# Performance work log

Measured on AMD Instinct MI355X. Metric: run time of the kernel, lower is better.

Reference implementation:

```python
import math
import jax, jax.numpy as jnp
import numpy as np

N_EXPERTS = 8
CAP_FACTOR = 1.25
D_MODEL = 1024
D_FF = 4096
B, T = 8, 2048


def setup_inputs() -> dict:
    key = jax.random.key(0)
    k1, k2, k3, k4 = jax.random.split(key, 4)
    hidden = jax.random.normal(k1, (B, T, D_MODEL), dtype=jnp.float32)
    # router: Linear(d_model, n_experts, bias=False), init std=0.01; store as (D, E)
    router_w = jax.random.normal(k2, (D_MODEL, N_EXPERTS), dtype=jnp.float32) * 0.01
    # per-expert MLP weights stacked: W1 (E, D, F), W2 (E, F, D)
    s1 = 1.0 / math.sqrt(D_MODEL)
    s2 = 1.0 / math.sqrt(D_FF)
    W1 = jax.random.uniform(k3, (N_EXPERTS, D_MODEL, D_FF), dtype=jnp.float32, minval=-s1, maxval=s1)
    W2 = jax.random.uniform(k4, (N_EXPERTS, D_FF, D_MODEL), dtype=jnp.float32, minval=-s2, maxval=s2)
    return {"hidden": hidden, "router_w": router_w, "W1": W1, "W2": W2}


def reference(hidden, router_w, W1, W2):
    Bb, Tt, D = hidden.shape
    N = Bb * Tt
    E = router_w.shape[1]
    capacity = min(int(math.ceil(CAP_FACTOR * N / E)), N)

    hidden_flat = hidden.reshape(N, D)
    logits = hidden_flat @ router_w                 # (N, E)
    router_probs = jax.nn.softmax(logits, axis=-1)  # (N, E)

    scores = router_probs.T                         # (E, N)
    weights, indices = jax.lax.top_k(scores, capacity)  # (E, C) each

    # gather tokens per expert: (E, C, D)
    expert_in = hidden_flat[indices]
    h = jnp.einsum('ecd,edf->ecf', expert_in, W1)
    h = jax.nn.gelu(h, approximate=False)           # torch nn.GELU default (erf)
    expert_out = jnp.einsum('ecf,efd->ecd', h, W2)  # (E, C, D)
    contrib = weights[..., None] * expert_out       # (E, C, D)

    output = jnp.zeros((N, D), dtype=hidden.dtype)
    output = output.at[indices.reshape(-1)].add(contrib.reshape(-1, D))
    output = output.reshape(Bb, Tt, D)

    eps = 1e-8
    entropy = -(router_probs * jnp.log(router_probs + eps)).sum(-1)
    aux_loss = -entropy.mean()
    return output, aux_loss
```

## Files before the change

### kernel.cpp

```cpp
#include <hip/hip_runtime.h>
#include <hip/hip_bf16.h>
#include <math.h>

#define NTOK 16384
#define DM 1024
#define DFF 4096
#define NEXP 8
#define CAP 2560

typedef __bf16 bf16;
typedef float f32x4 __attribute__((ext_vector_type(4)));
typedef bf16 bf16x8 __attribute__((ext_vector_type(8)));
typedef bf16 bf16x4 __attribute__((ext_vector_type(4)));

#define OFF_PROBS 0ull
#define OFF_IDX   524288ull
#define OFF_WTS   606208ull
#define OFF_W1T   688128ull
#define OFF_W2T   67796992ull
#define OFF_X     134905856ull
#define OFF_ENT   OFF_X
#define OFF_H     176848896ull
#define WS_MIN    197820416ull
#define WS_FUSED  344621056ull

#define BAR() do { asm volatile("" ::: "memory"); __builtin_amdgcn_s_barrier(); asm volatile("" ::: "memory"); } while (0)

__device__ __forceinline__ void gl16(const bf16* g, const bf16* l) {
  __builtin_amdgcn_global_load_lds((const __attribute__((address_space(1))) void*)g,
                                   (__attribute__((address_space(3))) void*)l, 16, 0, 0);
}

__device__ __forceinline__ float gelu_f(float x) {
  float u = 1.5957691216057308f * (x + 0.044715f * x * x * x);
  return x * __builtin_amdgcn_rcpf(1.f + __expf(-u));
}

__global__ __launch_bounds__(256) void k_transpose_cvt(const float* __restrict__ src,
                                                       bf16* __restrict__ dst, int R, int C) {
  __shared__ float tile[64][69];
  int e = blockIdx.z;
  src += (size_t)e * R * C;
  dst += (size_t)e * R * C;
  int c0 = blockIdx.x * 64, r0 = blockIdx.y * 64;
  int t = threadIdx.x;
  int tr = t >> 4, tc4 = (t & 15) * 4;
#pragma unroll
  for (int i = 0; i < 4; i++) {
    int r = tr + i * 16;
    float4 v = *(const float4*)(src + (size_t)(r0 + r) * C + c0 + tc4);
    tile[r][tc4] = v.x; tile[r][tc4 + 1] = v.y; tile[r][tc4 + 2] = v.z; tile[r][tc4 + 3] = v.w;
  }
  __syncthreads();
#pragma unroll
  for (int i = 0; i < 4; i++) {
    int orr = tr + i * 16;
    bf16x4 o = {(bf16)tile[tc4][orr], (bf16)tile[tc4 + 1][orr],
                (bf16)tile[tc4 + 2][orr], (bf16)tile[tc4 + 3][orr]};
    *(bf16x4*)(dst + (size_t)(c0 + orr) * R + r0 + tc4) = o;
  }
}

__global__ __launch_bounds__(256) void k_router(const float* __restrict__ hidden,
                                                const float* __restrict__ rw,
                                                float* __restrict__ probsT,
                                                float* __restrict__ entPart) {
  __shared__ float went[4];
  int wv = threadIdx.x >> 6, lane = threadIdx.x & 63;
  int token = blockIdx.x * 4 + wv;
  float acc[NEXP];
#pragma unroll
  for (int e = 0; e < NEXP; e++) acc[e] = 0.f;
  const float* hp = hidden + (size_t)token * DM;
  for (int d = lane; d < DM; d += 64) {
    float h = hp[d];
#pragma unroll
    for (int e = 0; e < NEXP; e++) acc[e] = fmaf(h, rw[d * NEXP + e], acc[e]);
  }
#pragma unroll
  for (int e = 0; e < NEXP; e++) {
    float v = acc[e];
#pragma unroll
    for (int s = 1; s < 64; s <<= 1) v += __shfl_xor(v, s);
    acc[e] = v;
  }
  float mx = acc[0];
#pragma unroll
  for (int e = 1; e < NEXP; e++) mx = fmaxf(mx, acc[e]);
  float p[NEXP], s = 0.f;
#pragma unroll
  for (int e = 0; e < NEXP; e++) { p[e] = expf(acc[e] - mx); s += p[e]; }
  float inv = 1.f / s;
  float ent = 0.f;
#pragma unroll
  for (int e = 0; e < NEXP; e++) { p[e] *= inv; ent += p[e] * logf(p[e] + 1e-8f); }
  if (lane < NEXP) probsT[(size_t)lane * NTOK + token] = p[lane];
  if (lane == 0) went[wv] = ent;
  __syncthreads();
  if (threadIdx.x == 0) entPart[blockIdx.x] = went[0] + went[1] + went[2] + went[3];
}

__global__ __launch_bounds__(256) void k_aux(const float* __restrict__ part, float* __restrict__ outAux) {
  __shared__ float s[256];
  int t = threadIdx.x;
  float v = 0.f;
#pragma unroll
  for (int i = 0; i < 16; i++) v += part[i * 256 + t];
  s[t] = v;
  __syncthreads();
  for (int st = 128; st > 0; st >>= 1) {
    if (t < st) s[t] += s[t + st];
    __syncthreads();
  }
  if (t == 0) outAux[0] = s[0] * (1.f / (float)NTOK);
}

__global__ __launch_bounds__(1024) void k_topk(const float* __restrict__ probsT,
                                               int* __restrict__ idx,
                                               float* __restrict__ wts) {
  int e = blockIdx.x;
  const float* row = probsT + (size_t)e * NTOK;
  int t = threadIdx.x;
  unsigned u[16];
#pragma unroll
  for (int j = 0; j < 16; j++) u[j] = __float_as_uint(row[j * 1024 + t]);
  __shared__ int wred[16];
  __shared__ int bc;
  __shared__ int cnt_gt, cnt_eq;
  __shared__ int eqbuf[2048];
  int lane = t & 63, wv = t >> 6;
  unsigned prefix = 0;
  for (int bit = 30; bit >= 0; bit--) {
    unsigned cand = prefix | (1u << bit);
    int c = 0;
#pragma unroll
    for (int j = 0; j < 16; j++) c += (u[j] >= cand) ? 1 : 0;
#pragma unroll
    for (int s = 1; s < 64; s <<= 1) c += __shfl_xor(c, s);
    if (lane == 0) wred[wv] = c;
    __syncthreads();
    if (t == 0) { int tot = 0; for (int k = 0; k < 16; k++) tot += wred[k]; bc = tot; }
    __syncthreads();
    if (bc >= CAP) prefix = cand;
  }
  unsigned vC = prefix;
  if (t == 0) { cnt_gt = 0; cnt_eq = 0; }
  __syncthreads();
#pragma unroll
  for (int j = 0; j < 16; j++) {
    int i = j * 1024 + t;
    if (u[j] > vC) {
      int p = atomicAdd(&cnt_gt, 1);
      idx[e * CAP + p] = i;
      wts[e * CAP + p] = __uint_as_float(u[j]);
    } else if (u[j] == vC) {
      int p = atomicAdd(&cnt_eq, 1);
      if (p < 2048) eqbuf[p] = i;
    }
  }
  __syncthreads();
  int m = cnt_gt;
  int ne = cnt_eq > 2048 ? 2048 : cnt_eq;
  int needed = CAP - m;
  for (int j = t; j < ne; j += 1024) {
    int my = eqbuf[j];
    int rank = 0;
    for (int k = 0; k < ne; k++) rank += (eqbuf[k] < my) ? 1 : 0;
    if (rank < needed) {
      idx[e * CAP + m + rank] = my;
      wts[e * CAP + m + rank] = __uint_as_float(vC);
    }
  }
}

__global__ void k_gather(const float* __restrict__ hidden, const int* __restrict__ idx,
                         bf16* __restrict__ X) {
  int ec = blockIdx.x;
  int token = idx[ec];
  const float4* src = (const float4*)(hidden + (size_t)token * DM);
  bf16* dstrow = X + (size_t)ec * DM;
  int t = threadIdx.x;
  float4 v = src[t];
  bf16x4 o = {(bf16)v.x, (bf16)v.y, (bf16)v.z, (bf16)v.w};
  *(bf16x4*)(dstrow + t * 4) = o;
}

template <int EPI>
__global__ __launch_bounds__(512, 2) void k_gemm256p(
    const bf16* __restrict__ Ab, const bf16* __restrict__ Bb,
    bf16* __restrict__ Hb, const int* __restrict__ idxb, const float* __restrict__ wtsb,
    float* __restrict__ outb, int serialE) {
  constexpr int KD = (EPI == 0) ? DM : DFF;
  constexpr int NT = (EPI == 0) ? 16 : 32;

  __shared__ bf16 As[2][256 * 64];
  __shared__ bf16 Bs[2][256 * 64];

  int e, slot, nA;
  if (serialE >= 0) { e = serialE; slot = blockIdx.x; nA = 1; }
  else {
    e = blockIdx.x & 7;
    slot = blockIdx.x >> 3;
    nA = (EPI == 0) ? 5 : ((slot < 16) ? 3 : 2);
  }
  const bf16* A = Ab + (size_t)e * ((EPI == 0) ? (size_t)CAP * DM : (size_t)CAP * DFF);
  const bf16* B = Bb + (size_t)e * ((EPI == 0) ? (size_t)DFF * DM : (size_t)DM * DFF);

  int t = threadIdx.x, lane = t & 63, wv = t >> 6;
  int wm = wv >> 2, wn = wv & 3;
  int l3 = lane >> 3, l7 = lane & 7;
  int cswz = (l7 ^ l3) * 8;

  auto decode = [&](int seq, int& m0, int& n0, int& k0) {
    int s_ = seq / 40, r_ = seq % 40;
    int bx = r_ >> 2, q = r_ & 3;
    m0 = bx * 256;
    if constexpr (EPI == 0) { n0 = (s_ * 4 + q) * 256; k0 = 0; }
    else { n0 = q * 256; k0 = s_ * 2048; }
  };

  auto stage = [&](const bf16* Am, const bf16* Bn, int half, int ktE, int buf) {
#pragma unroll
    for (int j = 0; j < 2; ++j) {
      int u = wv * 2 + j;
      int rb; const bf16* G; bf16* L;
      if (half == 0)      { rb = u * 8 + (u >> 3) * 64;            G = Am + (size_t)(rb + l3) * KD; L = &As[buf][rb * 64]; }
      else if (half == 3) { rb = 64 + u * 8 + (u >> 3) * 64;       G = Am + (size_t)(rb + l3) * KD; L = &As[buf][rb * 64]; }
      else if (half == 1) { rb = (u >> 2) * 64 + (u & 3) * 8;      G = Bn + (size_t)(rb + l3) * KD; L = &Bs[buf][rb * 64]; }
      else                { rb = (u >> 2) * 64 + 32 + (u & 3) * 8; G = Bn + (size_t)(rb + l3) * KD; L = &Bs[buf][rb * 64]; }
      gl16(G + ktE + cswz, L + lane * 8);
    }
  };

  auto rdA = [&](const bf16* base, int q, int i, int kk) -> bf16x8 {
    int rr = wm * 128 + (q * 4 + i) * 16 + (lane & 15);
    int slt = (kk * 4 + (lane >> 4)) ^ l7;
    return *(const bf16x8*)((const char*)base + rr * 128 + slt * 16);
  };
  auto rdB = [&](const bf16* base, int h, int i, int kk) -> bf16x8 {
    int rr = wn * 64 + (h * 2 + i) * 16 + (lane & 15);
    int slt = (kk * 4 + (lane >> 4)) ^ l7;
    return *(const bf16x8*)((const char*)base + rr * 128 + slt * 16);
  };

  f32x4 acc[8][4];
#pragma unroll
  for (int m = 0; m < 8; m++)
#pragma unroll
    for (int n = 0; n < 4; n++) acc[m][n] = (f32x4){0.f, 0.f, 0.f, 0.f};
  bf16x8 aF[4][2], bF0[2][2], bF1[2][2];

  int seq = slot;
  int m0, n0, k0;
  decode(seq, m0, n0, k0);
  const bf16* Am = A + (size_t)m0 * KD;
  const bf16* Bn = B + (size_t)n0 * KD;

  stage(Am, Bn, 0, k0, 0); stage(Am, Bn, 1, k0, 0);
  stage(Am, Bn, 2, k0, 0); stage(Am, Bn, 3, k0, 0);
  asm volatile("s_waitcnt vmcnt(4)" ::: "memory");
  BAR();

  for (int a = 0; a < nA; ++a) {
    int m0N = 0, n0N = 0, k0N = 0;
    const bf16 *AmN = nullptr, *BnN = nullptr;
    bool hasNextA = (a + 1 < nA);
    if (hasNextA) {
      decode(seq + 32, m0N, n0N, k0N);
      AmN = A + (size_t)m0N * KD;
      BnN = B + (size_t)n0N * KD;
    }
    for (int kt = 0; kt < NT; ++kt) {
      int cur = kt & 1;
      bool lastT = (kt == NT - 1);
      bool nl = !lastT || hasNextA;
      const bf16* sA = lastT ? AmN : Am;
      const bf16* sB = lastT ? BnN : Bn;
      int sk = lastT ? k0N : (k0 + (kt + 1) * 64);

#pragma unroll
      for (int i = 0; i < 4; i++)
#pragma unroll
        for (int kk = 0; kk < 2; kk++) aF[i][kk] = rdA(As[cur], 0, i, kk);
#pragma unroll
      for (int i = 0; i < 2; i++)
#pragma unroll
        for (int kk = 0; kk < 2; kk++) bF0[i][kk] = rdB(Bs[cur], 0, i, kk);
      if (nl) stage(sA, sB, 0, sk, cur ^ 1);
      BAR();
      asm volatile("s_waitcnt lgkmcnt(0)" ::: "memory");
      __builtin_amdgcn_s_setprio(1);
#pragma unroll
      for (int i = 0; i < 4; i++)
#pragma unroll
        for (int j = 0; j < 2; j++)
#pragma unroll
          for (int kk = 0; kk < 2; kk++)
            acc[i][j] = __builtin_amdgcn_mfma_f32_16x16x32_bf16(aF[i][kk], bF0[j][kk], acc[i][j], 0, 0, 0);
      __builtin_amdgcn_s_setprio(0);
      if (nl) asm volatile("s_waitcnt vmcnt(4)" ::: "memory");
      else    asm volatile("s_waitcnt vmcnt(2)" ::: "memory");
      BAR();
#pragma unroll
      for (int i = 0; i < 2; i++)
#pragma unroll
        for (int kk = 0; kk < 2; kk++) bF1[i][kk] = rdB(Bs[cur], 1, i, kk);
      if (nl) stage(sA, sB, 1, sk, cur ^ 1);
      BAR();
      asm volatile("s_waitcnt lgkmcnt(0)" ::: "memory");
      __builtin_amdgcn_s_setprio(1);
#pragma unroll
      for (int i = 0; i < 4; i++)
#pragma unroll
        for (int j = 0; j < 2; j++)
#pragma unroll
          for (int kk = 0; kk < 2; kk++)
            acc[i][2 + j] = __builtin_amdgcn_mfma_f32_16x16x32_bf16(aF[i][kk], bF1[j][kk], acc[i][2 + j], 0, 0, 0);
      __builtin_amdgcn_s_setprio(0);
      if (nl) asm volatile("s_waitcnt vmcnt(4)" ::: "memory");
      else    asm volatile("s_waitcnt vmcnt(0)" ::: "memory");
      BAR();
#pragma unroll
      for (int i = 0; i < 4; i++)
#pragma unroll
        for (int kk = 0; kk < 2; kk++) aF[i][kk] = rdA(As[cur], 1, i, kk);
      if (nl) stage(sA, sB, 2, sk, cur ^ 1);
      BAR();
      asm volatile("s_waitcnt lgkmcnt(0)" ::: "memory");
      __builtin_amdgcn_s_setprio(1);
#pragma unroll
      for (int i = 0; i < 4; i++)
#pragma unroll
        for (int j = 0; j < 2; j++)
#pragma unroll
          for (int kk = 0; kk < 2; kk++)
            acc[4 + i][j] = __builtin_amdgcn_mfma_f32_16x16x32_bf16(aF[i][kk], bF0[j][kk], acc[4 + i][j], 0, 0, 0);
      __builtin_amdgcn_s_setprio(0);
      BAR();
      if (nl) stage(sA, sB, 3, sk, cur ^ 1);
      BAR();
      __builtin_amdgcn_s_setprio(1);
#pragma unroll
      for (int i = 0; i < 4; i++)
#pragma unroll
        for (int j = 0; j < 2; j++)
#pragma unroll
          for (int kk = 0; kk < 2; kk++)
            acc[4 + i][2 + j] = __builtin_amdgcn_mfma_f32_16x16x32_bf16(aF[i][kk], bF1[j][kk], acc[4 + i][2 + j], 0, 0, 0);
      __builtin_amdgcn_s_setprio(0);
      if (nl) asm volatile("s_waitcnt vmcnt(4)" ::: "memory");
      BAR();
    }

    int cl = lane & 15, rg = (lane >> 4) * 4;
    if constexpr (EPI == 0) {
      bf16* He = Hb + (size_t)e * CAP * DFF;
#pragma unroll
      for (int m = 0; m < 8; m++) {
        int rowg = m0 + wm * 128 + m * 16 + rg;
#pragma unroll
        for (int n = 0; n < 4; n++) {
          int col = n0 + wn * 64 + n * 16 + cl;
#pragma unroll
          for (int rr = 0; rr < 4; rr++)
            He[(size_t)(rowg + rr) * DFF + col] = (bf16)gelu_f(acc[m][n][rr]);
        }
      }
    } else {
      const int* idxE = idxb + e * CAP;
      const float* wtsE = wtsb + e * CAP;
#pragma unroll
      for (int m = 0; m < 8; m++) {
        int rowg = m0 + wm * 128 + m * 16 + rg;
#pragma unroll
        for (int rr = 0; rr < 4; rr++) {
          int c = rowg + rr;
          int token = idxE[c];
          float w = wtsE[c];
          float* op = outb + (size_t)token * DM + n0 + wn * 64 + cl;
#pragma unroll
          for (int n = 0; n < 4; n++) atomicAdd(op + n * 16, w * acc[m][n][rr]);
        }
      }
    }
#pragma unroll
    for (int m = 0; m < 8; m++)
#pragma unroll
      for (int n = 0; n < 4; n++) acc[m][n] = (f32x4){0.f, 0.f, 0.f, 0.f};

    if (hasNextA) { m0 = m0N; n0 = n0N; k0 = k0N; Am = AmN; Bn = BnN; seq += 32; }
  }
}

extern "C" void kernel_launch(void* const* d_in, const int* in_sizes, int n_in,
                              void* d_out, int out_size, void* d_ws, size_t ws_size,
                              hipStream_t stream) {
  const float* hidden = (const float*)d_in[0];
  const float* router_w = (const float*)d_in[1];
  const float* W1 = (const float*)d_in[2];
  const float* W2 = (const float*)d_in[3];
  float* out = (float*)d_out;
  if (ws_size < WS_MIN) return;

  char* ws = (char*)d_ws;
  float* probsT = (float*)(ws + OFF_PROBS);
  int* idxb = (int*)(ws + OFF_IDX);
  float* wtsb = (float*)(ws + OFF_WTS);
  bf16* W1T = (bf16*)(ws + OFF_W1T);
  bf16* W2T = (bf16*)(ws + OFF_W2T);
  bf16* Xall = (bf16*)(ws + OFF_X);
  float* entPart = (float*)(ws + OFF_ENT);
  bf16* Hbuf = (bf16*)(ws + OFF_H);

  hipMemsetAsync(d_out, 0, (size_t)out_size * sizeof(float), stream);

  k_transpose_cvt<<<dim3(DFF / 64, DM / 64, NEXP), 256, 0, stream>>>(W1, W1T, DM, DFF);
  k_transpose_cvt<<<dim3(DM / 64, DFF / 64, NEXP), 256, 0, stream>>>(W2, W2T, DFF, DM);

  k_router<<<NTOK / 4, 256, 0, stream>>>(hidden, router_w, probsT, entPart);
  k_aux<<<1, 256, 0, stream>>>(entPart, out + (size_t)NTOK * DM);
  k_topk<<<NEXP, 1024, 0, stream>>>(probsT, idxb, wtsb);
  k_gather<<<NEXP * CAP, 256, 0, stream>>>(hidden, idxb, Xall);

  if (ws_size >= WS_FUSED) {
    k_gemm256p<0><<<256, 512, 0, stream>>>(Xall, W1T, Hbuf, nullptr, nullptr, nullptr, -1);
    k_gemm256p<1><<<256, 512, 0, stream>>>(Hbuf, W2T, nullptr, idxb, wtsb, out, -1);
  } else {
    for (int e = 0; e < NEXP; e++) {
      bf16* Hadj = Hbuf - (size_t)e * CAP * DFF;
      k_gemm256p<0><<<160, 512, 0, stream>>>(Xall, W1T, Hadj, nullptr, nullptr, nullptr, e);
      k_gemm256p<1><<<80, 512, 0, stream>>>(Hadj, W2T, nullptr, idxb, wtsb, out, e);
    }
  }
}
```

Baseline: 671.1 us.

## Split GEMM2 K into four chunks, use inline-asm LDS reads and sched barriers

The second GEMM now splits its K dimension of 4096 into four 1024-wide chunks rather than two 2048-wide ones. That gives 160 tiles per expert, so every block processes five tiles, matching GEMM1 and balancing the load (previously some blocks ran 3 tiles and others 2). LDS fragment reads switch to inline ds_read_b128 asm, and the memory clobbers are dropped from the barriers and waitcnts, with sched_barrier added so the compiler can schedule more freely. The risks are more atomic or split-K output accumulation traffic, and the weaker ordering of hand-placed waitcnts, which relies on the asm volatile ordering to stay correct.

```diff
diff --git a/kernel.cpp b/kernel.cpp
--- a/kernel.cpp
+++ b/kernel.cpp
@@ -24,11 +24,19 @@
 #define WS_MIN    197820416ull
 #define WS_FUSED  344621056ull
 
-#define BAR() do { asm volatile("" ::: "memory"); __builtin_amdgcn_s_barrier(); asm volatile("" ::: "memory"); } while (0)
+#define BAR() __builtin_amdgcn_s_barrier()
 
 __device__ __forceinline__ void gl16(const bf16* g, const bf16* l) {
   __builtin_amdgcn_global_load_lds((const __attribute__((address_space(1))) void*)g,
                                    (__attribute__((address_space(3))) void*)l, 16, 0, 0);
+}
+
+__device__ __forceinline__ bf16x8 ldsrd16(const bf16* a) {
+  bf16x8 d;
+  asm volatile("ds_read_b128 %0, %1"
+               : "=v"(d)
+               : "v"((const __attribute__((address_space(3))) bf16*)a));
+  return d;
 }
 
 __device__ __forceinline__ float gelu_f(float x) {
@@ -191,18 +199,14 @@
     bf16* __restrict__ Hb, const int* __restrict__ idxb, const float* __restrict__ wtsb,
     float* __restrict__ outb, int serialE) {
   constexpr int KD = (EPI == 0) ? DM : DFF;
-  constexpr int NT = (EPI == 0) ? 16 : 32;
+  constexpr int NT = 16;
 
   __shared__ bf16 As[2][256 * 64];
   __shared__ bf16 Bs[2][256 * 64];
 
   int e, slot, nA;
   if (serialE >= 0) { e = serialE; slot = blockIdx.x; nA = 1; }
-  else {
-    e = blockIdx.x & 7;
-    slot = blockIdx.x >> 3;
-    nA = (EPI == 0) ? 5 : ((slot < 16) ? 3 : 2);
-  }
+  else { e = blockIdx.x & 7; slot = blockIdx.x >> 3; nA = 5; }
   const bf16* A = Ab + (size_t)e * ((EPI == 0) ? (size_t)CAP * DM : (size_t)CAP * DFF);
   const bf16* B = Bb + (size_t)e * ((EPI == 0) ? (size_t)DFF * DM : (size_t)DM * DFF);
 
@@ -211,12 +215,11 @@
   int l3 = lane >> 3, l7 = lane & 7;
   int cswz = (l7 ^ l3) * 8;
 
-  auto decode = [&](int seq, int& m0, int& n0, int& k0) {
-    int s_ = seq / 40, r_ = seq % 40;
-    int bx = r_ >> 2, q = r_ & 3;
-    m0 = bx * 256;
-    if constexpr (EPI == 0) { n0 = (s_ * 4 + q) * 256; k0 = 0; }
-    else { n0 = q * 256; k0 = s_ * 2048; }
+  auto decode = [&](int sq, int& m0_, int& n0_, int& k0_) {
+    int s_ = sq / 40, r_ = sq % 40;
+    m0_ = (r_ >> 2) * 256;
+    if constexpr (EPI == 0) { n0_ = ((s_ << 2) + (r_ & 3)) * 256; k0_ = 0; }
+    else { n0_ = (r_ & 3) * 256; k0_ = s_ * 1024; }
   };
 
   auto stage = [&](const bf16* Am, const bf16* Bn, int half, int ktE, int buf) {
@@ -235,12 +238,12 @@
   auto rdA = [&](const bf16* base, int q, int i, int kk) -> bf16x8 {
     int rr = wm * 128 + (q * 4 + i) * 16 + (lane & 15);
     int slt = (kk * 4 + (lane >> 4)) ^ l7;
-    return *(const bf16x8*)((const char*)base + rr * 128 + slt * 16);
+    return ldsrd16((const bf16*)((const char*)base + rr * 128 + slt * 16));
   };
   auto rdB = [&](const bf16* base, int h, int i, int kk) -> bf16x8 {
     int rr = wn * 64 + (h * 2 + i) * 16 + (lane & 15);
     int slt = (kk * 4 + (lane >> 4)) ^ l7;
-    return *(const bf16x8*)((const char*)base + rr * 128 + slt * 16);
+    return ldsrd16((const bf16*)((const char*)base + rr * 128 + slt * 16));
   };
 
   f32x4 acc[8][4];
@@ -258,7 +261,7 @@
 
   stage(Am, Bn, 0, k0, 0); stage(Am, Bn, 1, k0, 0);
   stage(Am, Bn, 2, k0, 0); stage(Am, Bn, 3, k0, 0);
-  asm volatile("s_waitcnt vmcnt(4)" ::: "memory");
+  asm volatile("s_waitcnt vmcnt(4)");
   BAR();
 
   for (int a = 0; a < nA; ++a) {
@@ -288,7 +291,8 @@
         for (int kk = 0; kk < 2; kk++) bF0[i][kk] = rdB(Bs[cur], 0, i, kk);
       if (nl) stage(sA, sB, 0, sk, cur ^ 1);
       BAR();
-      asm volatile("s_waitcnt lgkmcnt(0)" ::: "memory");
+      asm volatile("s_waitcnt lgkmcnt(0)");
+      __builtin_amdgcn_sched_barrier(0);
       __builtin_amdgcn_s_setprio(1);
 #pragma unroll
       for (int i = 0; i < 4; i++)
@@ -298,8 +302,8 @@
           for (int kk = 0; kk < 2; kk++)
             acc[i][j] = __builtin_amdgcn_mfma_f32_16x16x32_bf16(aF[i][kk], bF0[j][kk], acc[i][j], 0, 0, 0);
       __builtin_amdgcn_s_setprio(0);
-      if (nl) asm volatile("s_waitcnt vmcnt(4)" ::: "memory");
-      else    asm volatile("s_waitcnt vmcnt(2)" ::: "memory");
+      if (nl) asm volatile("s_waitcnt vmcnt(4)");
+      else    asm volatile("s_waitcnt vmcnt(2)");
       BAR();
 #pragma unroll
       for (int i = 0; i < 2; i++)
@@ -307,7 +311,8 @@
         for (int kk = 0; kk < 2; kk++) bF1[i][kk] = rdB(Bs[cur], 1, i, kk);
       if (nl) stage(sA, sB, 1, sk, cur ^ 1);
       BAR();
-      asm volatile("s_waitcnt lgkmcnt(0)" ::: "memory");
+      asm volatile("s_waitcnt lgkmcnt(0)");
+      __builtin_amdgcn_sched_barrier(0);
       __builtin_amdgcn_s_setprio(1);
 #pragma unroll
       for (int i = 0; i < 4; i++)
@@ -317,8 +322,8 @@
           for (int kk = 0; kk < 2; kk++)
             acc[i][2 + j] = __builtin_amdgcn_mfma_f32_16x16x32_bf16(aF[i][kk], bF1[j][kk], acc[i][2 + j], 0, 0, 0);
       __builtin_amdgcn_s_setprio(0);
-      if (nl) asm volatile("s_waitcnt vmcnt(4)" ::: "memory");
-      else    asm volatile("s_waitcnt vmcnt(0)" ::: "memory");
+      if (nl) asm volatile("s_waitcnt vmcnt(4)");
+      else    asm volatile("s_waitcnt vmcnt(0)");
       BAR();
 #pragma unroll
       for (int i = 0; i < 4; i++)
@@ -326,7 +331,8 @@
         for (int kk = 0; kk < 2; kk++) aF[i][kk] = rdA(As[cur], 1, i, kk);
       if (nl) stage(sA, sB, 2, sk, cur ^ 1);
       BAR();
-      asm volatile("s_waitcnt lgkmcnt(0)" ::: "memory");
+      asm volatile("s_waitcnt lgkmcnt(0)");
+      __builtin_amdgcn_sched_barrier(0);
       __builtin_amdgcn_s_setprio(1);
 #pragma unroll
       for (int i = 0; i < 4; i++)
@@ -348,7 +354,7 @@
           for (int kk = 0; kk < 2; kk++)
             acc[4 + i][2 + j] = __builtin_amdgcn_mfma_f32_16x16x32_bf16(aF[i][kk], bF1[j][kk], acc[4 + i][2 + j], 0, 0, 0);
       __builtin_amdgcn_s_setprio(0);
-      if (nl) asm volatile("s_waitcnt vmcnt(4)" ::: "memory");
+      if (nl) asm volatile("s_waitcnt vmcnt(4)");
       BAR();
     }
 
@@ -429,7 +435,7 @@
     for (int e = 0; e < NEXP; e++) {
       bf16* Hadj = Hbuf - (size_t)e * CAP * DFF;
       k_gemm256p<0><<<160, 512, 0, stream>>>(Xall, W1T, Hadj, nullptr, nullptr, nullptr, e);
-      k_gemm256p<1><<<80, 512, 0, stream>>>(Hadj, W2T, nullptr, idxb, wtsb, out, e);
-    }
-  }
-}
+      k_gemm256p<1><<<160, 512, 0, stream>>>(Hadj, W2T, nullptr, idxb, wtsb, out, e);
+    }
+  }
+}
```

After: 718.0 us. +7.0%, slower.
